# Kernel optimization log

Measured on AMD Instinct MI355X. Metric: run time of the kernel, lower is better.

The kernel has to match this reference:

```python
import jax, jax.numpy as jnp
import numpy as np

NUM_GROUPS = 32
EPS = 1e-6


def setup_inputs() -> dict:
    key = jax.random.key(0)
    ks = jax.random.split(key, 11)
    b, c, h, w = 4, 512, 64, 64
    s = 0.02
    return {
        "x": jax.random.normal(ks[0], (b, c, h, w), dtype=jnp.float32),
        "gn_w": jnp.ones((c,), dtype=jnp.float32),
        "gn_b": jnp.zeros((c,), dtype=jnp.float32),
        "wq": jax.random.normal(ks[1], (c, c), dtype=jnp.float32) * s,
        "bq": jax.random.normal(ks[2], (c,), dtype=jnp.float32) * s,
        "wk": jax.random.normal(ks[3], (c, c), dtype=jnp.float32) * s,
        "bk": jax.random.normal(ks[4], (c,), dtype=jnp.float32) * s,
        "wv": jax.random.normal(ks[5], (c, c), dtype=jnp.float32) * s,
        "bv": jax.random.normal(ks[6], (c,), dtype=jnp.float32) * s,
        "wo": jax.random.normal(ks[7], (c, c), dtype=jnp.float32) * s,
        "bo": jax.random.normal(ks[8], (c,), dtype=jnp.float32) * s,
    }


def _group_norm(x, gamma, beta):
    b, c, h, w = x.shape
    g = NUM_GROUPS
    xg = x.reshape(b, g, c // g, h, w)
    mean = jnp.mean(xg, axis=(2, 3, 4), keepdims=True)
    var = jnp.var(xg, axis=(2, 3, 4), keepdims=True)
    xg = (xg - mean) * jax.lax.rsqrt(var + EPS)
    x = xg.reshape(b, c, h, w)
    return x * gamma[None, :, None, None] + beta[None, :, None, None]


def _conv1x1(x, wmat, bias):
    # x: [b,c,h,w], wmat: [out,in] -> [b,out,h,w]
    return jnp.einsum('bchw,oc->bohw', x, wmat) + bias[None, :, None, None]


def reference(x, gn_w, gn_b, wq, bq, wk, bk, wv, bv, wo, bo):
    b, c, h, w = x.shape
    h_ = _group_norm(x, gn_w, gn_b)
    q = _conv1x1(h_, wq, bq).reshape(b, c, h * w)  # [b,c,hw]
    k = _conv1x1(h_, wk, bk).reshape(b, c, h * w)
    v = _conv1x1(h_, wv, bv).reshape(b, c, h * w)
    scale = float(c) ** (-0.5)
    # scores[b,i,j] = sum_c q[b,c,i] * k[b,c,j]
    scores = jnp.einsum('bci,bcj->bij', q, k) * scale
    attn = jax.nn.softmax(scores, axis=2)  # softmax over j (keys)
    # out[b,c,i] = sum_j v[b,c,j] * attn[b,i,j]
    out = jnp.einsum('bcj,bij->bci', v, attn).reshape(b, c, h, w)
    out = _conv1x1(out, wo, bo)
    return x + out
```

## Files before the change

### kernel.cpp

```cpp
#include <hip/hip_runtime.h>
#include <math.h>

using short8 = __attribute__((ext_vector_type(8))) short;
using f32x4  = __attribute__((ext_vector_type(4))) float;
using i32x8  = __attribute__((ext_vector_type(8))) int;

__device__ __forceinline__ ushort f2bf(float f) {
    union { float f; uint u; } c; c.f = f;
    uint u = c.u;
    uint r = (u + 0x7FFFu + ((u >> 16) & 1u)) >> 16;
    return (ushort)r;
}
__device__ __forceinline__ unsigned char f2fp8(float x) {
    return (unsigned char)__builtin_amdgcn_cvt_pk_fp8_f32(x, 0.f, 0, false);
}
__device__ __forceinline__ uint pk4_fp8(float a, float b, float c, float d) {
    int v = __builtin_amdgcn_cvt_pk_fp8_f32(a, b, 0, false);
    v = __builtin_amdgcn_cvt_pk_fp8_f32(c, d, v, true);
    return (uint)v;
}

__device__ __forceinline__ void gload16(const void* g, void* l) {
    __builtin_amdgcn_global_load_lds(
        (const __attribute__((address_space(1))) unsigned int*)g,
        (__attribute__((address_space(3))) unsigned int*)l,
        16, 0, 0);
}

__global__ __launch_bounds__(256) void prep_weights(
    const float* __restrict__ wq, const float* __restrict__ bq,
    const float* __restrict__ wk, const float* __restrict__ bk,
    const float* __restrict__ wv, const float* __restrict__ wo,
    ushort* __restrict__ Wqk, ushort* __restrict__ Wv, ushort* __restrict__ Wo,
    float* __restrict__ bqk, float* __restrict__ stats, float scale)
{
    int idx = blockIdx.x * 256 + threadIdx.x;
    if (idx < 1024 * 512) {
        float v = (idx < 262144) ? wq[idx] * scale : wk[idx - 262144];
        Wqk[idx] = f2bf(v);
    }
    if (idx < 262144) {
        Wv[idx] = f2bf(wv[idx]);
        Wo[idx] = f2bf(wo[idx]);
    }
    if (idx < 1024) bqk[idx] = (idx < 512) ? bq[idx] * scale : bk[idx - 512];
    if (idx < 256) stats[idx] = 0.f;
}

__global__ __launch_bounds__(256) void gn_stats(
    const float* __restrict__ x, float* __restrict__ stats)
{
    int blk = blockIdx.x;
    int grp = blk >> 3, sub = blk & 7;
    const float* xp = x + (size_t)grp * 65536 + sub * 8192;
    int tid = threadIdx.x;

    float s = 0.f, sq = 0.f;
    #pragma unroll
    for (int j = 0; j < 8; ++j) {
        float4 v = *(const float4*)&xp[tid * 4 + j * 1024];
        s  += v.x + v.y + v.z + v.w;
        sq += v.x * v.x + v.y * v.y + v.z * v.z + v.w * v.w;
    }
    #pragma unroll
    for (int off = 32; off; off >>= 1) {
        s  += __shfl_xor(s,  off, 64);
        sq += __shfl_xor(sq, off, 64);
    }
    __shared__ float red[8];
    if ((tid & 63) == 0) { red[(tid >> 6) * 2] = s; red[(tid >> 6) * 2 + 1] = sq; }
    __syncthreads();
    if (tid == 0) {
        atomicAdd(&stats[grp * 2],     red[0] + red[2] + red[4] + red[6]);
        atomicAdd(&stats[grp * 2 + 1], red[1] + red[3] + red[5] + red[7]);
    }
}

__global__ __launch_bounds__(256) void gn_apply(
    const float* __restrict__ x, const float* __restrict__ gamma,
    const float* __restrict__ beta, const float* __restrict__ stats,
    ushort* __restrict__ hnt)
{
    int blk = blockIdx.x;
    int grp = blk >> 4, tile = blk & 15;
    int b = grp >> 5, g = grp & 31;
    const float* xp = x + (size_t)grp * 65536;
    int tid = threadIdx.x;

    float mean = stats[grp * 2] * (1.f / 65536.f);
    float var  = stats[grp * 2 + 1] * (1.f / 65536.f) - mean * mean;
    float rstd = rsqrtf(var + 1e-6f);

    int i0 = tile * 256;
    __shared__ ushort ls[16][256];
    #pragma unroll
    for (int ch = 0; ch < 16; ++ch) {
        float a = rstd * gamma[g * 16 + ch];
        float c = beta[g * 16 + ch] - mean * a;
        ls[ch][tid] = f2bf(xp[ch * 4096 + i0 + tid] * a + c);
    }
    __syncthreads();
    ushort t[16];
    #pragma unroll
    for (int ch = 0; ch < 16; ++ch) t[ch] = ls[ch][tid];
    size_t dst = ((size_t)b * 4096 + i0 + tid) * 512 + g * 16;
    *(uint4*)&hnt[dst]     = *(const uint4*)&t[0];
    *(uint4*)&hnt[dst + 8] = *(const uint4*)&t[8];
}

template <int BIAS, int OUT>
__global__ __launch_bounds__(256, 4) void gemm_nt(
    const ushort* __restrict__ Ag, const ushort* __restrict__ Bg,
    void* __restrict__ Cv, void* __restrict__ Cv2,
    const float* __restrict__ bias, const float* __restrict__ resid,
    int N, int K, int lda, int ldb,
    long sA, long sB, long sC)
{
    const int bz = blockIdx.z;
    Ag += (size_t)bz * sA;
    Bg += (size_t)bz * sB;

    const int tid  = threadIdx.x;
    const int wave = tid >> 6, lane = tid & 63;
    const int q = lane >> 4, lr = lane & 15;
    const int m0 = blockIdx.x * 128, n0 = blockIdx.y * 128;
    const int wm = (wave >> 1) * 64, wn = (wave & 1) * 64;

    __shared__ __align__(16) ushort As[2][128 * 32];
    __shared__ __align__(16) ushort Bs[2][128 * 32];

    const int srow = wave * 32 + (lane >> 2);
    const int skc  = (lane & 3) << 3;
    const size_t aoff0 = (size_t)(m0 + srow) * lda + skc;
    const size_t aoff1 = aoff0 + (size_t)16 * lda;
    const size_t boff0 = (size_t)(n0 + srow) * ldb + skc;
    const size_t boff1 = boff0 + (size_t)16 * ldb;
    const int l0 = wave * 1024, l1 = wave * 1024 + 512;

    f32x4 acc[4][4] = {};

    for (int kb = 0; kb < K; kb += 64) {
        __syncthreads();
        gload16(&Ag[aoff0 + kb],      &As[0][l0]);
        gload16(&Ag[aoff1 + kb],      &As[0][l1]);
        gload16(&Ag[aoff0 + kb + 32], &As[1][l0]);
        gload16(&Ag[aoff1 + kb + 32], &As[1][l1]);
        gload16(&Bg[boff0 + kb],      &Bs[0][l0]);
        gload16(&Bg[boff1 + kb],      &Bs[0][l1]);
        gload16(&Bg[boff0 + kb + 32], &Bs[1][l0]);
        gload16(&Bg[boff1 + kb + 32], &Bs[1][l1]);
        __syncthreads();

        #pragma unroll
        for (int kh = 0; kh < 2; ++kh) {
            short8 af[4], bfr[4];
            #pragma unroll
            for (int mt = 0; mt < 4; ++mt)
                af[mt] = *(const short8*)&As[kh][(wm + mt * 16 + lr) * 32 + q * 8];
            #pragma unroll
            for (int nt = 0; nt < 4; ++nt)
                bfr[nt] = *(const short8*)&Bs[kh][(wn + nt * 16 + lr) * 32 + q * 8];
            #pragma unroll
            for (int mt = 0; mt < 4; ++mt)
                #pragma unroll
                for (int nt = 0; nt < 4; ++nt)
                    acc[mt][nt] = __builtin_amdgcn_mfma_f32_16x16x32_bf16(
                        af[mt], bfr[nt], acc[mt][nt], 0, 0, 0);
        }
    }

    if (OUT == 2) {
        __syncthreads();
        unsigned char* C8 = (unsigned char*)&As[0][0];
        const int ch = (wn >> 4) + (lr >> 2);
        const int cb = (lr & 3) * 4;
        #pragma unroll
        for (int mt = 0; mt < 4; ++mt) {
            #pragma unroll
            for (int t = 0; t < 4; ++t) {
                int row = wm + mt * 16 + q * 4 + t;
                float b = (BIAS == 1) ? bias[m0 + row] : 0.f;
                uint d = pk4_fp8(acc[mt][0][t] + b, acc[mt][1][t] + b,
                                 acc[mt][2][t] + b, acc[mt][3][t] + b);
                *(uint*)&C8[row * 128 + (((ch ^ (row & 7)) << 4) | cb)] = d;
            }
        }
        __syncthreads();
        const int er = tid >> 3, eck = tid & 7;
        unsigned char* obase = (unsigned char*)Cv + (size_t)bz * sC
                             + (size_t)blockIdx.y * 65536 + (size_t)m0 * 128;
        #pragma unroll
        for (int p = 0; p < 4; ++p) {
            int row = p * 32 + er;
            uint4 v = *(const uint4*)&C8[row * 128 + ((eck ^ (row & 7)) << 4)];
            *(uint4*)&obase[(size_t)row * 128 + eck * 16] = v;
        }
        return;
    }

    if (OUT == 3) {
        __syncthreads();
        unsigned char* C8 = (unsigned char*)&As[0][0];
        #pragma unroll
        for (int mt = 0; mt < 4; ++mt) {
            #pragma unroll
            for (int nt = 0; nt < 4; ++nt) {
                int col = wn + nt * 16 + lr;
                #pragma unroll
                for (int t = 0; t < 4; ++t) {
                    int row = wm + mt * 16 + q * 4 + t;
                    float v = acc[mt][nt][t];
                    if (BIAS == 1) v += bias[m0 + row];
                    if (BIAS == 2) v += bias[n0 + col];
                    if (n0 < 512) v *= 16.f;
                    C8[row * 128 + ((((col >> 4) ^ (row & 7)) << 4) | (col & 15))]
                        = f2fp8(v);
                }
            }
        }
        __syncthreads();
        const int er = tid >> 3, eck = tid & 7;
        #pragma unroll
        for (int p = 0; p < 4; ++p) {
            int row = p * 32 + er;
            uint4 v = *(const uint4*)&C8[row * 128 + ((eck ^ (row & 7)) << 4)];
            if (n0 < 512)
                *(uint4*)&((unsigned char*)Cv)[(size_t)bz * sC
                    + (size_t)(m0 + row) * 512 + n0 + eck * 16] = v;
            else
                *(uint4*)&((unsigned char*)Cv2)[(size_t)bz * sC
                    + (size_t)(m0 + row) * 512 + (n0 - 512) + eck * 16] = v;
        }
        return;
    }

    #pragma unroll
    for (int mt = 0; mt < 4; ++mt) {
        int rb = m0 + wm + mt * 16 + q * 4;
        #pragma unroll
        for (int nt = 0; nt < 4; ++nt) {
            int cn = n0 + wn + nt * 16 + lr;
            #pragma unroll
            for (int t = 0; t < 4; ++t) {
                int r = rb + t;
                float v = acc[mt][nt][t];
                if (BIAS == 1) v += bias[r];
                if (BIAS == 2) v += bias[cn];
                if (OUT == 1) {
                    size_t o = (size_t)bz * sC + (size_t)r * N + cn;
                    ((float*)Cv)[o] = v + resid[o];
                } else {
                    size_t o = (size_t)bz * sC + (size_t)r * N + cn;
                    ((ushort*)Cv)[o] = f2bf(v);
                }
            }
        }
    }
}

__global__ __launch_bounds__(256, 4) void gemm_qk(
    const unsigned char* __restrict__ Q8, const unsigned char* __restrict__ K8,
    unsigned char* __restrict__ P8, float* __restrict__ Zpart)
{
    const int bz = blockIdx.z;
    const unsigned char* Ag = Q8 + (size_t)bz * 2097152;
    const unsigned char* Bg = K8 + (size_t)bz * 2097152;

    const int tid  = threadIdx.x;
    const int wave = tid >> 6, lane = tid & 63;
    const int q = lane >> 4, lr = lane & 15;
    int L = blockIdx.y * 32 + blockIdx.x;
    L = (L & 7) * 128 + (L >> 3);
    const int bx = L & 31, by = L >> 5;
    const int m0 = bx * 128, n0 = by * 128;
    const int wm = (wave >> 1) * 64, wn = (wave & 1) * 64;

    __shared__ __align__(16) unsigned char smem[32768];
    unsigned char* As = smem;
    unsigned char* Bs = smem + 16384;
    unsigned char* C8 = smem;
    float* Zs = (float*)Bs;

    const int lrow = lane >> 3;
    const size_t laneoff = (size_t)lrow * 512 + ((lane & 7) ^ (lrow & 7)) * 16;
    const size_t abase = (size_t)(m0 + wave * 32) * 512 + laneoff;
    const size_t bbase = (size_t)(n0 + wave * 32) * 512 + laneoff;
    unsigned char* lA = As + wave * 32 * 128;
    unsigned char* lB = Bs + wave * 32 * 128;

    const int e0 = (2 * q) ^ (lr & 7), e1 = e0 ^ 1;

    f32x4 acc[4][4] = {};
    const int sA = 0x7B7B7B7B;
    const int sB = 0x7F7F7F7F;

    for (int kb = 0; kb < 512; kb += 128) {
        __syncthreads();
        #pragma unroll
        for (int t = 0; t < 4; ++t) {
            gload16(Ag + abase + (size_t)t * 4096 + kb, lA + t * 1024);
            gload16(Bg + bbase + (size_t)t * 4096 + kb, lB + t * 1024);
        }
        __syncthreads();

        i32x8 af[4], bf[4];
        #pragma unroll
        for (int mt = 0; mt < 4; ++mt) {
            int r = wm + mt * 16 + lr;
            union { uint4 v[2]; i32x8 f; } u;
            u.v[0] = *(const uint4*)&As[r * 128 + e0 * 16];
            u.v[1] = *(const uint4*)&As[r * 128 + e1 * 16];
            af[mt] = u.f;
        }
        #pragma unroll
        for (int nt = 0; nt < 4; ++nt) {
            int r = wn + nt * 16 + lr;
            union { uint4 v[2]; i32x8 f; } u;
            u.v[0] = *(const uint4*)&Bs[r * 128 + e0 * 16];
            u.v[1] = *(const uint4*)&Bs[r * 128 + e1 * 16];
            bf[nt] = u.f;
        }
        #pragma unroll
        for (int mt = 0; mt < 4; ++mt)
            #pragma unroll
            for (int nt = 0; nt < 4; ++nt)
                acc[mt][nt] = __builtin_amdgcn_mfma_scale_f32_16x16x128_f8f6f4(
                    af[mt], bf[nt], acc[mt][nt], 0, 0, 0, sA, 0, sB);
    }

    float rs[4][4];
    uint  pd[4][4];
    #pragma unroll
    for (int mt = 0; mt < 4; ++mt) {
        #pragma unroll
        for (int t = 0; t < 4; ++t) {
            float e0v = __expf(acc[mt][0][t]) * 32.f;
            float e1v = __expf(acc[mt][1][t]) * 32.f;
            float e2v = __expf(acc[mt][2][t]) * 32.f;
            float e3v = __expf(acc[mt][3][t]) * 32.f;
            rs[mt][t] = (e0v + e1v) + (e2v + e3v);
            pd[mt][t] = pk4_fp8(e0v, e1v, e2v, e3v);
        }
    }

    __syncthreads();
    const int ch = (wn >> 4) + (lr >> 2);
    const int cb = (lr & 3) * 4;
    #pragma unroll
    for (int mt = 0; mt < 4; ++mt) {
        #pragma unroll
        for (int t = 0; t < 4; ++t) {
            int row = wm + mt * 16 + q * 4 + t;
            *(uint*)&C8[row * 128 + (((ch ^ (row & 7)) << 4) | cb)] = pd[mt][t];
            Zs[((wave & 1) * 128 + row) * 16 + lr] = rs[mt][t];
        }
    }
    __syncthreads();
    if (tid < 128) {
        const float4* z0 = (const float4*)&Zs[tid * 16];
        const float4* z1 = (const float4*)&Zs[2048 + tid * 16];
        float4 a0 = z0[0], a1 = z0[1], a2 = z0[2], a3 = z0[3];
        float4 b0 = z1[0], b1 = z1[1], b2 = z1[2], b3 = z1[3];
        float z = ((a0.x + a0.y + a0.z + a0.w) + (a1.x + a1.y + a1.z + a1.w))
                + ((a2.x + a2.y + a2.z + a2.w) + (a3.x + a3.y + a3.z + a3.w))
                + ((b0.x + b0.y + b0.z + b0.w) + (b1.x + b1.y + b1.z + b1.w))
                + ((b2.x + b2.y + b2.z + b2.w) + (b3.x + b3.y + b3.z + b3.w));
        Zpart[(size_t)bz * 131072 + (size_t)by * 4096 + m0 + tid] = z;
    }
    const int er = tid >> 3, eck = tid & 7;
    unsigned char* obase = P8 + (size_t)bz * 16777216
                         + (size_t)by * 524288 + (size_t)m0 * 128;
    #pragma unroll
    for (int p = 0; p < 4; ++p) {
        int row = p * 32 + er;
        uint4 v = *(const uint4*)&C8[row * 128 + ((eck ^ (row & 7)) << 4)];
        *(uint4*)&obase[(size_t)row * 128 + eck * 16] = v;
    }
}

__global__ __launch_bounds__(256, 4) void gemm_pv(
    const unsigned char* __restrict__ P8, const unsigned char* __restrict__ V8,
    ushort* __restrict__ Ot, const float* __restrict__ Zpart)
{
    const int bz = blockIdx.z;
    const unsigned char* Ag = P8 + (size_t)bz * 16777216;
    const unsigned char* Bg = V8 + (size_t)bz * 2097152;

    const int tid  = threadIdx.x;
    const int wave = tid >> 6, lane = tid & 63;
    const int q = lane >> 4, lr = lane & 15;
    const int m0 = blockIdx.x * 128, n0 = blockIdx.y * 128;
    const int wm = (wave >> 1) * 64, wn = (wave & 1) * 64;

    __shared__ __align__(16) unsigned char smem[32768];
    __shared__ float Zr[128];
    unsigned char* As = smem;
    unsigned char* Bs = smem + 16384;
    ushort* Cs = (ushort*)smem;

    if (tid < 128) {
        const float* zp = Zpart + (size_t)bz * 131072 + m0 + tid;
        float z = 0.f;
        #pragma unroll
        for (int by = 0; by < 32; ++by) z += zp[by * 4096];
        Zr[tid] = 1.0f / z;
    }

    const int lrow = lane >> 3;
    const int swz = ((lane & 7) ^ (lrow & 7)) * 16;
    const size_t abase = (size_t)(m0 + wave * 32 + lrow) * 128 + swz;
    const size_t bbase = (size_t)(n0 + wave * 32 + lrow) * 128 + swz;
    unsigned char* lA = As + wave * 32 * 128;
    unsigned char* lB = Bs + wave * 32 * 128;

    const int e0 = (2 * q) ^ (lr & 7), e1 = e0 ^ 1;

    f32x4 acc[4][4] = {};
    const int sA = 0x7F7F7F7F;
    const int sB = 0x7F7F7F7F;

    for (int kt = 0; kt < 32; ++kt) {
        __syncthreads();
        #pragma unroll
        for (int t = 0; t < 4; ++t) {
            gload16(Ag + (size_t)kt * 524288 + abase + t * 1024, lA + t * 1024);
            gload16(Bg + (size_t)kt * 65536  + bbase + t * 1024, lB + t * 1024);
        }
        __syncthreads();

        i32x8 af[4], bf[4];
        #pragma unroll
        for (int mt = 0; mt < 4; ++mt) {
            int r = wm + mt * 16 + lr;
            union { uint4 v[2]; i32x8 f; } u;
            u.v[0] = *(const uint4*)&As[r * 128 + e0 * 16];
            u.v[1] = *(const uint4*)&As[r * 128 + e1 * 16];
            af[mt] = u.f;
        }
        #pragma unroll
        for (int nt = 0; nt < 4; ++nt) {
            int r = wn + nt * 16 + lr;
            union { uint4 v[2]; i32x8 f; } u;
            u.v[0] = *(const uint4*)&Bs[r * 128 + e0 * 16];
            u.v[1] = *(const uint4*)&Bs[r * 128 + e1 * 16];
            bf[nt] = u.f;
        }
        #pragma unroll
        for (int mt = 0; mt < 4; ++mt)
            #pragma unroll
            for (int nt = 0; nt < 4; ++nt)
                acc[mt][nt] = __builtin_amdgcn_mfma_scale_f32_16x16x128_f8f6f4(
                    af[mt], bf[nt], acc[mt][nt], 0, 0, 0, sA, 0, sB);
    }

    __syncthreads();
    #pragma unroll
    for (int mt = 0; mt < 4; ++mt) {
        #pragma unroll
        for (int t = 0; t < 4; ++t) {
            int row = wm + mt * 16 + q * 4 + t;
            float iz = Zr[row];
            #pragma unroll
            for (int nt = 0; nt < 4; ++nt) {
                int col = wn + nt * 16 + lr;
                Cs[row * 128 + ((((col >> 3) ^ (row & 7)) << 3) | (col & 7))]
                    = f2bf(acc[mt][nt][t] * iz);
            }
        }
    }
    __syncthreads();
    const int er = tid >> 4, eck = tid & 15;
    ushort* orow = Ot + (size_t)bz * 2097152 + (size_t)m0 * 512 + n0;
    #pragma unroll
    for (int p = 0; p < 8; ++p) {
        int row = p * 16 + er;
        uint4 v = *(const uint4*)&Cs[row * 128 + ((eck ^ (row & 7)) << 3)];
        *(uint4*)&orow[(size_t)row * 512 + eck * 8] = v;
    }
}

extern "C" void kernel_launch(void* const* d_in, const int* in_sizes, int n_in,
                              void* d_out, int out_size, void* d_ws, size_t ws_size,
                              hipStream_t stream)
{
    const float* x   = (const float*)d_in[0];
    const float* gnw = (const float*)d_in[1];
    const float* gnb = (const float*)d_in[2];
    const float* wq  = (const float*)d_in[3];
    const float* bq  = (const float*)d_in[4];
    const float* wk  = (const float*)d_in[5];
    const float* bk  = (const float*)d_in[6];
    const float* wv  = (const float*)d_in[7];
    const float* bv  = (const float*)d_in[8];
    const float* wo  = (const float*)d_in[9];
    const float* bo  = (const float*)d_in[10];
    float* out = (float*)d_out;

    char* ws = (char*)d_ws;
    unsigned char* P8  = (unsigned char*)(ws);
    ushort*        Ot  = (ushort*)(ws + 67108864);
    ushort*        hnt = (ushort*)(ws + 83886080);
    unsigned char* Q8  = (unsigned char*)(ws + 100663296);
    unsigned char* K8  = (unsigned char*)(ws + 109051904);
    unsigned char* V8  = (unsigned char*)(ws + 117440512);
    float*         Zp  = (float*) (ws + 125829120);
    ushort*        Wqk = (ushort*)(ws + 127926272);
    ushort*        Wv  = (ushort*)(ws + 128974848);
    ushort*        Wo  = (ushort*)(ws + 129499136);
    float*         bqk = (float*) (ws + 130023424);
    float*         st  = (float*) (ws + 130027520);

    const float scale = 1.0f / sqrtf(512.0f);
    const long sHW  = 512L * 4096;

    prep_weights<<<2048, 256, 0, stream>>>(wq, bq, wk, bk, wv, wo,
                                           Wqk, Wv, Wo, bqk, st, scale);
    gn_stats<<<1024, 256, 0, stream>>>(x, st);
    gn_apply<<<2048, 256, 0, stream>>>(x, gnw, gnb, st, hnt);

    gemm_nt<2, 3><<<dim3(32, 8, 4), 256, 0, stream>>>(
        hnt, Wqk, Q8, K8, bqk, nullptr,
        1024, 512, 512, 512, sHW, 0L, sHW);

    gemm_nt<1, 2><<<dim3(4, 32, 4), 256, 0, stream>>>(
        Wv, hnt, V8, nullptr, bv, nullptr,
        4096, 512, 512, 512, 0L, sHW, sHW);

    gemm_qk<<<dim3(32, 32, 4), 256, 0, stream>>>(Q8, K8, P8, Zp);

    gemm_pv<<<dim3(32, 4, 4), 256, 0, stream>>>(P8, V8, Ot, Zp);

    gemm_nt<1, 1><<<dim3(4, 32, 4), 256, 0, stream>>>(
        Wo, Ot, out, nullptr, bo, x,
        4096, 512, 512, 512, 0L, sHW, sHW);
}
```

Measured before the change: 269.7 us.

## Double-buffer LDS tiles in gemm_pv to overlap loads with MFMA

```diff
diff --git a/kernel.cpp b/kernel.cpp
--- a/kernel.cpp
+++ b/kernel.cpp
@@ -378,7 +378,7 @@
     }
 }
 
-__global__ __launch_bounds__(256, 4) void gemm_pv(
+__global__ __launch_bounds__(256, 2) void gemm_pv(
     const unsigned char* __restrict__ P8, const unsigned char* __restrict__ V8,
     ushort* __restrict__ Ot, const float* __restrict__ Zpart)
 {
@@ -392,11 +392,10 @@
     const int m0 = blockIdx.x * 128, n0 = blockIdx.y * 128;
     const int wm = (wave >> 1) * 64, wn = (wave & 1) * 64;
 
-    __shared__ __align__(16) unsigned char smem[32768];
+    __shared__ __align__(16) unsigned char As[2][16384];
+    __shared__ __align__(16) unsigned char Bs[2][16384];
     __shared__ float Zr[128];
-    unsigned char* As = smem;
-    unsigned char* Bs = smem + 16384;
-    ushort* Cs = (ushort*)smem;
+    ushort* Cs = (ushort*)&As[0][0];
 
     if (tid < 128) {
         const float* zp = Zpart + (size_t)bz * 131072 + m0 + tid;
@@ -410,8 +409,7 @@
     const int swz = ((lane & 7) ^ (lrow & 7)) * 16;
     const size_t abase = (size_t)(m0 + wave * 32 + lrow) * 128 + swz;
     const size_t bbase = (size_t)(n0 + wave * 32 + lrow) * 128 + swz;
-    unsigned char* lA = As + wave * 32 * 128;
-    unsigned char* lB = Bs + wave * 32 * 128;
+    const int lws = wave * 4096;
 
     const int e0 = (2 * q) ^ (lr & 7), e1 = e0 ^ 1;
 
@@ -419,30 +417,38 @@
     const int sA = 0x7F7F7F7F;
     const int sB = 0x7F7F7F7F;
 
+    auto stage = [&](int kt, int buf) {
+        #pragma unroll
+        for (int t = 0; t < 4; ++t) {
+            gload16(Ag + (size_t)kt * 524288 + abase + t * 1024,
+                    &As[buf][lws + t * 1024]);
+            gload16(Bg + (size_t)kt * 65536  + bbase + t * 1024,
+                    &Bs[buf][lws + t * 1024]);
+        }
+    };
+
+    stage(0, 0);
+    __syncthreads();
+
     for (int kt = 0; kt < 32; ++kt) {
-        __syncthreads();
-        #pragma unroll
-        for (int t = 0; t < 4; ++t) {
-            gload16(Ag + (size_t)kt * 524288 + abase + t * 1024, lA + t * 1024);
-            gload16(Bg + (size_t)kt * 65536  + bbase + t * 1024, lB + t * 1024);
-        }
-        __syncthreads();
+        const int cur = kt & 1;
+        if (kt < 31) stage(kt + 1, cur ^ 1);
 
         i32x8 af[4], bf[4];
         #pragma unroll
         for (int mt = 0; mt < 4; ++mt) {
             int r = wm + mt * 16 + lr;
             union { uint4 v[2]; i32x8 f; } u;
-            u.v[0] = *(const uint4*)&As[r * 128 + e0 * 16];
-            u.v[1] = *(const uint4*)&As[r * 128 + e1 * 16];
+            u.v[0] = *(const uint4*)&As[cur][r * 128 + e0 * 16];
+            u.v[1] = *(const uint4*)&As[cur][r * 128 + e1 * 16];
             af[mt] = u.f;
         }
         #pragma unroll
         for (int nt = 0; nt < 4; ++nt) {
             int r = wn + nt * 16 + lr;
             union { uint4 v[2]; i32x8 f; } u;
-            u.v[0] = *(const uint4*)&Bs[r * 128 + e0 * 16];
-            u.v[1] = *(const uint4*)&Bs[r * 128 + e1 * 16];
+            u.v[0] = *(const uint4*)&Bs[cur][r * 128 + e0 * 16];
+            u.v[1] = *(const uint4*)&Bs[cur][r * 128 + e1 * 16];
             bf[nt] = u.f;
         }
         #pragma unroll
@@ -451,9 +457,10 @@
             for (int nt = 0; nt < 4; ++nt)
                 acc[mt][nt] = __builtin_amdgcn_mfma_scale_f32_16x16x128_f8f6f4(
                     af[mt], bf[nt], acc[mt][nt], 0, 0, 0, sA, 0, sB);
-    }
-
-    __syncthreads();
+
+        __syncthreads();
+    }
+
     #pragma unroll
     for (int mt = 0; mt < 4; ++mt) {
         #pragma unroll
```

Measured after the change: 271.3 us. No clear change (+0.6%).
